# Performance work log

Hardware: AMD Instinct MI355X
Metric: run time of the kernel (lower is better)

The kernel has to match this reference:

```python
import jax, jax.numpy as jnp
import numpy as np

N = 2097152   # number of points
TDIM = 16     # t_feat dim
HID = 64      # map_st hidden
BIG = 10000.0 # outer-bin extension from get_xy_compute


def setup_inputs() -> dict:
    key = jax.random.key(0)
    ks = jax.random.split(key, 4)
    x = jax.random.normal(ks[0], (N, 3), dtype=jnp.float32)
    t_feat = jax.random.normal(ks[1], (N, TDIM), dtype=jnp.float32)
    mask = jnp.array([1.0, 1.0, 0.0], dtype=jnp.float32)
    W1 = jax.random.normal(ks[2], (2 + TDIM, HID), dtype=jnp.float32) * 0.1
    b1 = jnp.zeros((HID,), dtype=jnp.float32)
    W2 = jax.random.normal(ks[3], (HID, 10), dtype=jnp.float32) * 0.1
    b2 = jnp.zeros((10,), dtype=jnp.float32)
    return {"x": x, "t_feat": t_feat, "mask": mask,
            "W1": W1, "b1": b1, "W2": W2, "b2": b2}


def _map_st(a, t, W1, b1, W2, b2):
    # a: [N,2] tanh of masked channels; t: [N,TDIM] -> [N,10] positive params
    z = jnp.concatenate([a, t], axis=-1)
    h = jax.nn.relu(z @ W1 + b1)
    return jax.nn.softplus(h @ W2 + b2) + 1e-4


def _get_xy(d):
    # d: [N,10] = dxl2,dxl1,dxr1,dxr2,dyl2,dyl1,dyr1,dyr2,kl,kr  (split order in get_all_xy)
    dxl2, dxl1, dxr1, dxr2 = d[..., 0], d[..., 1], d[..., 2], d[..., 3]
    dyl2, dyl1, dyr1, dyr2 = d[..., 4], d[..., 5], d[..., 6], d[..., 7]
    kl, kr = d[..., 8] * 2.0, d[..., 9] * 2.0
    xL1 = -dxl1;            yL1 = -dyl1
    xL2 = -dxl1 - dxl2;     yL2 = -dyl1 - dyl2
    xR1 = dxr1;             yR1 = dyr1
    xR2 = dxr1 + dxr2;      yR2 = dyr1 + dyr2
    xR3 = xR2 + BIG;        yR3 = yR2 + kr * BIG
    xL3 = xL2 - BIG;        yL3 = yL2 - kl * BIG
    all_x = jnp.stack([xL3, xL2, xL1, xR1, xR2, xR3], axis=-1)  # [N,6] monotonic
    all_y = jnp.stack([yL3, yL2, yL1, yR1, yR2, yR3], axis=-1)
    return all_x, all_y


def _interp(xk, yk, qx):
    # xk,yk: [N,6] knots; qx: [N]. Piecewise-linear interpolation (InterpGrad.forw_compute out).
    xl, xr = xk[..., :-1], xk[..., 1:]
    yl, yr = yk[..., :-1], yk[..., 1:]
    qx = jnp.clip(qx, xl[..., 0] * 0.99, xr[..., -1] * 0.99)
    q = qx[..., None]                       # [N,1]
    in_range = (q >= xl) & (q < xr)         # exactly one bin per row after clamp
    vals = (yr - yl) / (xr - xl) * (q - xl) + yl
    return jnp.sum(jnp.where(in_range, vals, 0.0), axis=-1)


def reference(x, t_feat, mask, W1, b1, W2, b2):
    # mask = [1,1,0]: channels 0,1 condition; channel 2 is transformed
    y_base = x * mask
    a = jnp.tanh(x[..., :2])
    d = _map_st(a, t_feat, W1, b1, W2, b2)
    all_x, all_y = _get_xy(d)
    out = _interp(all_x, all_y, x[..., 2])  # [N]
    return jnp.concatenate([y_base[..., :2], out[..., None]], axis=-1)
```

## Files before the change

### kernel.cpp

```cpp
#include <hip/hip_runtime.h>
#include <hip/hip_bf16.h>

typedef __attribute__((ext_vector_type(8))) short bf16x8;
typedef __attribute__((ext_vector_type(4))) float f32x4;
typedef __attribute__((ext_vector_type(4))) int   i32x4;

#define BIGC 10000.0f
#define TPW 4
#define WAVES 4

__device__ __forceinline__ float fast_exp2(float x) { return __builtin_amdgcn_exp2f(x); }
__device__ __forceinline__ float fast_log2(float x) { return __builtin_amdgcn_logf(x); }
__device__ __forceinline__ float fast_rcp(float x)  { return __builtin_amdgcn_rcpf(x); }

__device__ __forceinline__ float fast_tanh(float x) {
    const float ax = fabsf(x);
    const float e  = fast_exp2(ax * 2.8853900817779268f);
    const float r  = 1.0f - 2.0f * fast_rcp(e + 1.0f);
    return copysignf(r, x);
}
__device__ __forceinline__ float fast_softplus(float v) {
    const float e = fast_exp2(fabsf(v) * -1.4426950408889634f);
    const float l = fast_log2(1.0f + e) * 0.6931471805599453f;
    return fmaxf(v, 0.0f) + l;
}
__device__ __forceinline__ unsigned pack2bf(float hi, float lo) {
    const unsigned uh = __builtin_bit_cast(unsigned, hi) + 0x8000u;
    const unsigned ul = __builtin_bit_cast(unsigned, lo) + 0x8000u;
    return __builtin_amdgcn_perm(uh, ul, 0x07060302u);
}

__global__ void __launch_bounds__(256) coupling_mfma3(
    const float* __restrict__ x, const float* __restrict__ t_feat,
    const float* __restrict__ mask, const float* __restrict__ W1,
    const float* __restrict__ b1, const float* __restrict__ W2,
    const float* __restrict__ b2, float* __restrict__ out, int n)
{
    __shared__ float lds_d[WAVES][64][11];

    const int wave = threadIdx.x >> 6;
    const int lane = threadIdx.x & 63;
    const int m    = lane & 15;
    const int q    = lane >> 4;
    const long nl  = n;

    bf16x8 w1f[4];
#pragma unroll
    for (int a = 0; a < 4; ++a) {
        float wv[8];
#pragma unroll
        for (int j = 0; j < 8; ++j) {
            const int k = q * 8 + j;
            const int col = 16 * a + m;
            float v = 0.0f;
            if (k < 16)       v = W1[(k + 2) * 64 + col];
            else if (k == 16) v = W1[0 * 64 + col];
            else if (k == 17) v = W1[1 * 64 + col];
            else if (k == 18) v = b1[col];
            wv[j] = v;
        }
        i32x4 f = { (int)pack2bf(wv[1], wv[0]), (int)pack2bf(wv[3], wv[2]),
                    (int)pack2bf(wv[5], wv[4]), (int)pack2bf(wv[7], wv[6]) };
        w1f[a] = __builtin_bit_cast(bf16x8, f);
    }
    bf16x8 w2f[2];
#pragma unroll
    for (int fi = 0; fi < 2; ++fi) {
        float wv[8];
#pragma unroll
        for (int j = 0; j < 8; ++j) {
            const int hid = 32 * fi + 16 * (j >> 2) + 4 * q + (j & 3);
            wv[j] = (m < 10) ? W2[hid * 10 + m] : 0.0f;
        }
        i32x4 f = { (int)pack2bf(wv[1], wv[0]), (int)pack2bf(wv[3], wv[2]),
                    (int)pack2bf(wv[5], wv[4]), (int)pack2bf(wv[7], wv[6]) };
        w2f[fi] = __builtin_bit_cast(bf16x8, f);
    }
    const float bias2 = (m < 10) ? b2[m] : 0.0f;
    const float m0 = mask[0], m1 = mask[1];

    for (int it = 0; it < TPW; ++it) {
        const long p0 = ((long)blockIdx.x * TPW + it) * (WAVES * 64) + wave * 64;

#pragma unroll
        for (int s = 0; s < 4; ++s) {
            const long prow = min(p0 + 16 * s + m, nl - 1);

            i32x4 zw = { 0, 0, 0, 0 };
            if (q < 2) {
                const float* tr = t_feat + prow * 16 + q * 8;
                const float4 t0 = ((const float4*)tr)[0];
                const float4 t1 = ((const float4*)tr)[1];
                zw[0] = (int)pack2bf(t0.y, t0.x);
                zw[1] = (int)pack2bf(t0.w, t0.z);
                zw[2] = (int)pack2bf(t1.y, t1.x);
                zw[3] = (int)pack2bf(t1.w, t1.z);
            } else if (q == 2) {
                const float* xr = x + prow * 3;
                zw[0] = (int)pack2bf(fast_tanh(xr[1]), fast_tanh(xr[0]));
                zw[1] = 0x3F80;
            }
            const bf16x8 zf = __builtin_bit_cast(bf16x8, zw);

            f32x4 acc[4];
#pragma unroll
            for (int a = 0; a < 4; ++a) {
                f32x4 c = { 0.0f, 0.0f, 0.0f, 0.0f };
                acc[a] = __builtin_amdgcn_mfma_f32_16x16x32_bf16(w1f[a], zf, c, 0, 0, 0);
            }

            float rl[16];
#pragma unroll
            for (int a = 0; a < 4; ++a)
#pragma unroll
                for (int r = 0; r < 4; ++r)
                    rl[4 * a + r] = fmaxf(acc[a][r], 0.0f);
            i32x4 a20 = { (int)pack2bf(rl[1],  rl[0]),  (int)pack2bf(rl[3],  rl[2]),
                          (int)pack2bf(rl[5],  rl[4]),  (int)pack2bf(rl[7],  rl[6]) };
            i32x4 a21 = { (int)pack2bf(rl[9],  rl[8]),  (int)pack2bf(rl[11], rl[10]),
                          (int)pack2bf(rl[13], rl[12]), (int)pack2bf(rl[15], rl[14]) };

            f32x4 cb = { bias2, bias2, bias2, bias2 };
            f32x4 cz = { 0.0f, 0.0f, 0.0f, 0.0f };
            f32x4 cd0 = __builtin_amdgcn_mfma_f32_16x16x32_bf16(
                            __builtin_bit_cast(bf16x8, a20), w2f[0], cb, 0, 0, 0);
            f32x4 cd1 = __builtin_amdgcn_mfma_f32_16x16x32_bf16(
                            __builtin_bit_cast(bf16x8, a21), w2f[1], cz, 0, 0, 0);

#pragma unroll
            for (int r = 0; r < 4; ++r) {
                const float dv = fast_softplus(cd0[r] + cd1[r]) + 0.0001f;
                if (m < 10) lds_d[wave][16 * s + 4 * q + r][m] = dv;
            }
        }

        const long p = p0 + lane;
        if (p < nl) {
            const float* dd = lds_d[wave][lane];
            const float dxl2 = dd[0], dxl1 = dd[1], dxr1 = dd[2], dxr2 = dd[3];
            const float dyl2 = dd[4], dyl1 = dd[5], dyr1 = dd[6], dyr2 = dd[7];
            const float kl = dd[8] * 2.0f, kr = dd[9] * 2.0f;

            const float xL1 = -dxl1,        yL1 = -dyl1;
            const float xL2 = -dxl1 - dxl2, yL2 = -dyl1 - dyl2;
            const float xR1 = dxr1,         yR1 = dyr1;
            const float xR2 = dxr1 + dxr2,  yR2 = dyr1 + dyr2;
            const float xR3 = xR2 + BIGC,   yR3 = fmaf(kr, BIGC, yR2);
            const float xL3 = xL2 - BIGC,   yL3 = fmaf(-kl, BIGC, yL2);

            const float* xr = x + p * 3;
            const float x0v = xr[0], x1v = xr[1], x2v = xr[2];

            float qx = fminf(fmaxf(x2v, xL3 * 0.99f), xR3 * 0.99f);
            float xl = xL3, xrr = xL2, yl = yL3, yr = yL2;
            if (qx >= xL2) { xl = xL2; xrr = xL1; yl = yL2; yr = yL1; }
            if (qx >= xL1) { xl = xL1; xrr = xR1; yl = yL1; yr = yR1; }
            if (qx >= xR1) { xl = xR1; xrr = xR2; yl = yR1; yr = yR2; }
            if (qx >= xR2) { xl = xR2; xrr = xR3; yl = yR2; yr = yR3; }
            const float slope = (yr - yl) * fast_rcp(xrr - xl);
            const float res = fmaf(slope, qx - xl, yl);

            out[p * 3 + 0] = x0v * m0;
            out[p * 3 + 1] = x1v * m1;
            out[p * 3 + 2] = res;
        }
    }
}

extern "C" void kernel_launch(void* const* d_in, const int* in_sizes, int n_in,
                              void* d_out, int out_size, void* d_ws, size_t ws_size,
                              hipStream_t stream) {
    const float* x      = (const float*)d_in[0];
    const float* t_feat = (const float*)d_in[1];
    const float* mask   = (const float*)d_in[2];
    const float* W1     = (const float*)d_in[3];
    const float* b1     = (const float*)d_in[4];
    const float* W2     = (const float*)d_in[5];
    const float* b2     = (const float*)d_in[6];
    float* out = (float*)d_out;

    const int n = in_sizes[0] / 3;
    const int pts_per_block = TPW * WAVES * 64;
    const int grid = (n + pts_per_block - 1) / pts_per_block;
    coupling_mfma3<<<grid, 256, 0, stream>>>(x, t_feat, mask, W1, b1, W2, b2, out, n);
}
```

Measured before the change: 264.4 us.

## Prefetch t_feat and x per tile, share tanh via bpermute, use hardware bf16 pack

Each 64-point tile now issues all t_feat float4 loads and the x loads up front, before the MFMA loop, and reuses the x values for the interpolation and output instead of reloading them. tanh is computed once per lane and moved to the q==2 lanes with ds_bpermute, replacing the redundant per-subtile tanh. pack2bf now uses the v_cvt_pk_bf16_f32 instruction, which rounds differently from the old add-and-truncate trick. Indices become 32-bit, tile bases are clamped so the last tile overlaps earlier points, and launch bounds request 4 blocks per CU. Holding the prefetched loads live in registers costs more VGPRs.

```diff
diff --git a/kernel.cpp b/kernel.cpp
--- a/kernel.cpp
+++ b/kernel.cpp
@@ -25,12 +25,12 @@
     return fmaxf(v, 0.0f) + l;
 }
 __device__ __forceinline__ unsigned pack2bf(float hi, float lo) {
-    const unsigned uh = __builtin_bit_cast(unsigned, hi) + 0x8000u;
-    const unsigned ul = __builtin_bit_cast(unsigned, lo) + 0x8000u;
-    return __builtin_amdgcn_perm(uh, ul, 0x07060302u);
-}
-
-__global__ void __launch_bounds__(256) coupling_mfma3(
+    unsigned r;
+    asm("v_cvt_pk_bf16_f32 %0, %1, %2" : "=v"(r) : "v"(lo), "v"(hi));
+    return r;
+}
+
+__global__ void __launch_bounds__(256, 4) coupling_mfma4(
     const float* __restrict__ x, const float* __restrict__ t_feat,
     const float* __restrict__ mask, const float* __restrict__ W1,
     const float* __restrict__ b1, const float* __restrict__ W2,
@@ -42,7 +42,7 @@
     const int lane = threadIdx.x & 63;
     const int m    = lane & 15;
     const int q    = lane >> 4;
-    const long nl  = n;
+    const int m4   = m << 2;
 
     bf16x8 w1f[4];
 #pragma unroll
@@ -80,24 +80,40 @@
     const float m0 = mask[0], m1 = mask[1];
 
     for (int it = 0; it < TPW; ++it) {
-        const long p0 = ((long)blockIdx.x * TPW + it) * (WAVES * 64) + wave * 64;
+        int pb = (blockIdx.x * TPW + it) * (WAVES * 64) + wave * 64;
+        pb = min(pb, n - 64);
+        pb = max(pb, 0);
+
+        const int pl  = pb + lane;
+        const int plc = min(pl, n - 1);
+        const float* xp = x + plc * 3;
+        const float xi0 = xp[0], xi1 = xp[1], xi2 = xp[2];
+
+        float4 ta[4], tb[4];
+        if (q < 2) {
+#pragma unroll
+            for (int s = 0; s < 4; ++s) {
+                const int ps = min(pb + 16 * s + m, n - 1);
+                const float4* tr = (const float4*)(t_feat + ps * 16 + q * 8);
+                ta[s] = tr[0];
+                tb[s] = tr[1];
+            }
+        }
+
+        const unsigned pk = pack2bf(fast_tanh(xi1), fast_tanh(xi0));
 
 #pragma unroll
         for (int s = 0; s < 4; ++s) {
-            const long prow = min(p0 + 16 * s + m, nl - 1);
+            const int tp = __builtin_amdgcn_ds_bpermute(s * 64 + m4, (int)pk);
 
             i32x4 zw = { 0, 0, 0, 0 };
             if (q < 2) {
-                const float* tr = t_feat + prow * 16 + q * 8;
-                const float4 t0 = ((const float4*)tr)[0];
-                const float4 t1 = ((const float4*)tr)[1];
-                zw[0] = (int)pack2bf(t0.y, t0.x);
-                zw[1] = (int)pack2bf(t0.w, t0.z);
-                zw[2] = (int)pack2bf(t1.y, t1.x);
-                zw[3] = (int)pack2bf(t1.w, t1.z);
+                zw[0] = (int)pack2bf(ta[s].y, ta[s].x);
+                zw[1] = (int)pack2bf(ta[s].w, ta[s].z);
+                zw[2] = (int)pack2bf(tb[s].y, tb[s].x);
+                zw[3] = (int)pack2bf(tb[s].w, tb[s].z);
             } else if (q == 2) {
-                const float* xr = x + prow * 3;
-                zw[0] = (int)pack2bf(fast_tanh(xr[1]), fast_tanh(xr[0]));
+                zw[0] = tp;
                 zw[1] = 0x3F80;
             }
             const bf16x8 zf = __builtin_bit_cast(bf16x8, zw);
@@ -134,8 +150,7 @@
             }
         }
 
-        const long p = p0 + lane;
-        if (p < nl) {
+        {
             const float* dd = lds_d[wave][lane];
             const float dxl2 = dd[0], dxl1 = dd[1], dxr1 = dd[2], dxr2 = dd[3];
             const float dyl2 = dd[4], dyl1 = dd[5], dyr1 = dd[6], dyr2 = dd[7];
@@ -148,10 +163,7 @@
             const float xR3 = xR2 + BIGC,   yR3 = fmaf(kr, BIGC, yR2);
             const float xL3 = xL2 - BIGC,   yL3 = fmaf(-kl, BIGC, yL2);
 
-            const float* xr = x + p * 3;
-            const float x0v = xr[0], x1v = xr[1], x2v = xr[2];
-
-            float qx = fminf(fmaxf(x2v, xL3 * 0.99f), xR3 * 0.99f);
+            float qx = fminf(fmaxf(xi2, xL3 * 0.99f), xR3 * 0.99f);
             float xl = xL3, xrr = xL2, yl = yL3, yr = yL2;
             if (qx >= xL2) { xl = xL2; xrr = xL1; yl = yL2; yr = yL1; }
             if (qx >= xL1) { xl = xL1; xrr = xR1; yl = yL1; yr = yR1; }
@@ -160,9 +172,12 @@
             const float slope = (yr - yl) * fast_rcp(xrr - xl);
             const float res = fmaf(slope, qx - xl, yl);
 
-            out[p * 3 + 0] = x0v * m0;
-            out[p * 3 + 1] = x1v * m1;
-            out[p * 3 + 2] = res;
+            if (pl < n) {
+                float* op = out + pl * 3;
+                op[0] = xi0 * m0;
+                op[1] = xi1 * m1;
+                op[2] = res;
+            }
         }
     }
 }
@@ -182,5 +197,5 @@
     const int n = in_sizes[0] / 3;
     const int pts_per_block = TPW * WAVES * 64;
     const int grid = (n + pts_per_block - 1) / pts_per_block;
-    coupling_mfma3<<<grid, 256, 0, stream>>>(x, t_feat, mask, W1, b1, W2, b2, out, n);
-}
+    coupling_mfma4<<<grid, 256, 0, stream>>>(x, t_feat, mask, W1, b1, W2, b2, out, n);
+}
```

Measured after the change: 235.6 us. 1.12x faster.
